# Kernel optimization log

Measured on AMD Instinct MI355X. Metric: run time of the kernel, lower is better.

The kernel has to match this reference:

```python
import jax, jax.numpy as jnp
import numpy as np

RADIUS = 1.3
COARSE = 64
FINE = 2
N_ATOMS = 64
SH_DIM = 9
DATA_DIM = SH_DIM * 3 + 1  # 28
N_INTRS = COARSE * 3 * 2 * FINE  # 768
STEP = (RADIUS * 2.0 / COARSE / FINE) / 2.0
BATCH = 1024


def sh_basis(d):
    # real spherical harmonics basis, degree 2 (9 coeffs), on normalized dirs
    d = d / jnp.linalg.norm(d, axis=-1, keepdims=True)
    x, y, z = d[..., 0], d[..., 1], d[..., 2]
    C0 = 0.28209479177387814
    C1 = 0.4886025119029199
    C20, C21, C22, C23, C24 = (1.0925484305920792, -1.0925484305920792,
                               0.31539156525252005, -1.0925484305920792,
                               0.5462742152960396)
    return jnp.stack([
        C0 * jnp.ones_like(x), -C1 * y, C1 * z, -C1 * x,
        C20 * x * y, C21 * y * z, C22 * (2.0 * z * z - x * x - y * y),
        C23 * x * z, C24 * (x * x - y * y)
    ], axis=-1)


def dict_interp(grid, atoms, pts):
    # l2_interp_v2: coarse-voxel dictionary coeffs x trilinear fine-atom interp
    # pts: [P,3] in [0,1)
    P = pts.shape[0]
    pc = pts * COARSE
    c = jnp.clip(jnp.floor(pc), 0, COARSE - 1).astype(jnp.int32)
    local = pc - c.astype(pts.dtype)  # position inside coarse voxel, [0,1)
    clin = (c[:, 0] * COARSE + c[:, 1]) * COARSE + c[:, 2]
    coeff = grid[clin]                              # [P, A]
    # project dictionary coeffs through atoms for every fine cell: [P, FINE^3, D]
    proj = jnp.einsum('pa,fad->pfd', coeff, atoms)
    u = local * FINE - 0.5
    f = jnp.floor(u)
    t = u - f
    i0 = jnp.clip(f, 0, FINE - 1).astype(jnp.int32)
    i1 = jnp.clip(f + 1.0, 0, FINE - 1).astype(jnp.int32)
    idx = jnp.stack([i0, i1], axis=-1)              # [P,3,2]
    w = jnp.stack([1.0 - t, t], axis=-1)            # [P,3,2]
    rows = jnp.arange(P)
    out = jnp.zeros((P, DATA_DIM), dtype=pts.dtype)
    for kx in (0, 1):
        for ky in (0, 1):
            for kz in (0, 1):
                lin = (idx[:, 0, kx] * FINE + idx[:, 1, ky]) * FINE + idx[:, 2, kz]
                wgt = w[:, 0, kx] * w[:, 1, ky] * w[:, 2, kz]
                out = out + wgt[:, None] * proj[rows, lin]
    return out


def _forward(rays_o, rays_d, grid, atoms):
    dt = rays_o.dtype
    # ---- sample_proposal (no grad) ----
    off_pos = (RADIUS - rays_o) / rays_d
    off_neg = (-RADIUS - rays_o) / rays_d
    start = jnp.max(jnp.minimum(off_pos, off_neg), axis=-1, keepdims=True)
    intersections = jax.lax.stop_gradient(
        start + jnp.arange(N_INTRS, dtype=dt)[None, :] * STEP)  # [B, 768]
    tr = intersections[:, :-1]  # [B, 767]
    pts = rays_o[:, None, :] + tr[..., None] * rays_d[:, None, :]  # [B,n,3]
    mask = jnp.all((pts > -RADIUS) & (pts < RADIUS), axis=-1)      # [B,n]
    pts = jax.lax.stop_gradient(pts)
    B, n = tr.shape
    # normalized coords in [0,1); masked-out points are clipped then zeroed later
    p = jnp.clip((pts + RADIUS) / (2.0 * RADIUS), 0.0, 1.0 - 1e-6).reshape(-1, 3)
    data = dict_interp(grid, atoms, p).reshape(B, n, DATA_DIM)
    # masked_scatter of sigma <=> dense compute + where(mask, ., 0)
    sigma = jnp.where(mask, jax.nn.relu(data[..., -1]), 0.0)
    dists = (intersections[:, 1:] - intersections[:, :-1]) * \
        jnp.linalg.norm(rays_d, axis=-1, keepdims=True)
    alpha = 1.0 - jnp.exp(-sigma * dists)
    trans = jnp.cumprod(1.0 - alpha + 1e-10, axis=-1)
    trans = jnp.concatenate([jnp.ones_like(trans[:, :1]), trans[:, :-1]], axis=-1)
    abs_light = alpha * trans  # per-sample weights
    sh_mult = sh_basis(rays_d)                      # [B, 9]
    sh = data[..., :-1].reshape(B, n, 3, SH_DIM)
    rgb_samp = jnp.einsum('bnck,bk->bnc', sh, sh_mult)
    rgb_samp = jax.nn.sigmoid(jnp.where(mask[..., None], rgb_samp, 0.0))
    comp = jnp.sum(abs_light[..., None] * rgb_samp, axis=1)  # [B,3]
    acc = jnp.sum(abs_light, axis=1)
    rgb = comp + (1.0 - acc)[:, None]  # white background
    depth = jnp.sum(abs_light * tr, axis=1)
    return rgb, alpha, depth


def setup_inputs():
    key = jax.random.key(0)
    k0, k1, k2, k3 = jax.random.split(key, 4)
    o = jax.random.normal(k0, (BATCH, 3), dtype=jnp.float32)
    o = o / jnp.linalg.norm(o, axis=-1, keepdims=True) * 2.5
    d = -o + 0.3 * jax.random.normal(k1, (BATCH, 3), dtype=jnp.float32)
    d = d / jnp.linalg.norm(d, axis=-1, keepdims=True)
    grid = 0.01 * jax.random.normal(k2, (COARSE ** 3, N_ATOMS), dtype=jnp.float32)
    atoms_sh = jax.random.uniform(k3, (FINE ** 3, N_ATOMS, DATA_DIM - 1), dtype=jnp.float32)
    atoms = jnp.concatenate(
        [atoms_sh, jnp.full((FINE ** 3, N_ATOMS, 1), 0.01, dtype=jnp.float32)], axis=-1)
    return {"rays_o": o, "rays_d": d, "grid": grid, "atoms": atoms, "grid_id": 0}


def reference(rays_o, rays_d, grid, atoms, grid_id):
    # grid_id selects among num_scenes grids; num_scenes=1 so grid is pre-selected
    return _forward(rays_o, rays_d, grid, atoms)
```

## Files before the change

kernel.cpp:

```cpp
#include <hip/hip_runtime.h>
#include <hip/hip_bf16.h>

#define RADIUS_F 1.3f
#define NSAMP 767
#define STEPF 0.01015625f
#define BATCH 1024
#define NWAVES 8
#define TPW 6

typedef __attribute__((ext_vector_type(8))) short short8;
typedef __attribute__((ext_vector_type(4))) float floatx4;

static __device__ __forceinline__ unsigned pkbf(float a, float b) {
    union { __hip_bfloat162 h; unsigned u; } cvt;
    cvt.h = __float22bfloat162_rn(make_float2(a, b));
    return cvt.u;
}

static __device__ __forceinline__ float coset4_sum(float p) {
    int q4 = __builtin_amdgcn_update_dpp(0, __float_as_int(p), 0x124, 0xf, 0xf, true);
    p = p + __int_as_float(q4);
    int q8 = __builtin_amdgcn_update_dpp(0, __float_as_int(p), 0x128, 0xf, 0xf, true);
    return p + __int_as_float(q8);
}

__launch_bounds__(512, 2)
__global__ void plenoxels_fwd(const float* __restrict__ rays_o,
                              const float* __restrict__ rays_d,
                              const float* __restrict__ grid,
                              const float* __restrict__ atoms,
                              float* __restrict__ out)
{
    __shared__ __align__(16) __hip_bfloat16 BpL[32 * 64];
    __shared__ __align__(16) float WL[NWAVES][16 * 12];
    __shared__ __align__(16) __hip_bfloat16 alphaL[768];
    __shared__ __align__(16) __hip_bfloat16 rgbL[768 * 3];

    const int tid  = threadIdx.x;
    const int ray  = blockIdx.x;
    const int lane = tid & 63;
    const int w    = tid >> 6;
    const int m    = lane & 15;
    const int quad = lane >> 4;

    const float ox = rays_o[ray * 3 + 0], oy = rays_o[ray * 3 + 1], oz = rays_o[ray * 3 + 2];
    const float dx = rays_d[ray * 3 + 0], dy = rays_d[ray * 3 + 1], dz = rays_d[ray * 3 + 2];

    float start;
    {
        float a0 = (RADIUS_F - ox) / dx, b0 = (-RADIUS_F - ox) / dx;
        float a1 = (RADIUS_F - oy) / dy, b1 = (-RADIUS_F - oy) / dy;
        float a2 = (RADIUS_F - oz) / dz, b2 = (-RADIUS_F - oz) / dz;
        start = fmaxf(fminf(a0, b0), fmaxf(fminf(a1, b1), fminf(a2, b2)));
    }
    const float dnorm = sqrtf(dx * dx + dy * dy + dz * dz);
    const float dist = STEPF * dnorm;

    float shm[9];
    {
        float inv = 1.0f / dnorm;
        float nx = dx * inv, ny = dy * inv, nz = dz * inv;
        shm[0] = 0.28209479177387814f;
        shm[1] = -0.4886025119029199f * ny;
        shm[2] = 0.4886025119029199f * nz;
        shm[3] = -0.4886025119029199f * nx;
        shm[4] = 1.0925484305920792f * nx * ny;
        shm[5] = -1.0925484305920792f * ny * nz;
        shm[6] = 0.31539156525252005f * (2.f * nz * nz - nx * nx - ny * ny);
        shm[7] = -1.0925484305920792f * nx * nz;
        shm[8] = 0.5462742152960396f * (nx * nx - ny * ny);
    }

    auto geom = [&](int s, float4& WA, float4& WB, int& clin) {
        float tr = start + (float)s * STEPF;
        float px = ox + tr * dx, py = oy + tr * dy, pz = oz + tr * dz;
        int mask = (px > -RADIUS_F) & (px < RADIUS_F) &
                   (py > -RADIUS_F) & (py < RADIUS_F) &
                   (pz > -RADIUS_F) & (pz < RADIUS_F);
        float maskf = mask ? 1.f : 0.f;
        const float sc = 1.0f / (2.0f * RADIUS_F);
        float qx = fminf(fmaxf((px + RADIUS_F) * sc, 0.f), 1.0f - 1e-6f);
        float qy = fminf(fmaxf((py + RADIUS_F) * sc, 0.f), 1.0f - 1e-6f);
        float qz = fminf(fmaxf((pz + RADIUS_F) * sc, 0.f), 1.0f - 1e-6f);
        float pcx = qx * 64.f, pcy = qy * 64.f, pcz = qz * 64.f;
        float cx = fminf(floorf(pcx), 63.f);
        float cy = fminf(floorf(pcy), 63.f);
        float cz = fminf(floorf(pcz), 63.f);
        float lx = pcx - cx, ly = pcy - cy, lz = pcz - cz;
        clin = (((int)cx * 64) + (int)cy) * 64 + (int)cz;
        float xw0, xw1, yw0, yw1, zw0, zw1;
        {
            float u = lx * 2.f - 0.5f, fF = floorf(u), t = u - fF;
            xw0 = (fF < 0.f) ? 1.f : ((fF > 0.f) ? 0.f : 1.f - t);
            xw1 = (fF < 0.f) ? 0.f : ((fF > 0.f) ? 1.f : t);
        }
        {
            float u = ly * 2.f - 0.5f, fF = floorf(u), t = u - fF;
            yw0 = (fF < 0.f) ? 1.f : ((fF > 0.f) ? 0.f : 1.f - t);
            yw1 = (fF < 0.f) ? 0.f : ((fF > 0.f) ? 1.f : t);
        }
        {
            float u = lz * 2.f - 0.5f, fF = floorf(u), t = u - fF;
            zw0 = (fF < 0.f) ? 1.f : ((fF > 0.f) ? 0.f : 1.f - t);
            zw1 = (fF < 0.f) ? 0.f : ((fF > 0.f) ? 1.f : t);
        }
        xw0 *= maskf; xw1 *= maskf;
        WA = make_float4(xw0 * yw0 * zw0, xw0 * yw0 * zw1, xw0 * yw1 * zw0, xw0 * yw1 * zw1);
        WB = make_float4(xw1 * yw0 * zw0, xw1 * yw0 * zw1, xw1 * yw1 * zw0, xw1 * yw1 * zw1);
    };

    const float4* g4 = (const float4*)grid;

    float4 WAc, WBc; int clinC;
    geom(w * (TPW * 16) + m, WAc, WBc, clinC);
    float4 cv0, cv1, cv2, cv3;
    {
        const float4* gp = g4 + (clinC << 4) + (quad << 2);
        cv0 = gp[0]; cv1 = gp[1]; cv2 = gp[2]; cv3 = gp[3];
    }

    for (int idx = tid; idx < 2048; idx += 512) {
        int col = idx >> 6, a = idx & 63;
        int f = col >> 2, c = col & 3;
        const float* base = atoms + (f * 64 + a) * 28;
        float sv;
        if (c == 3) sv = base[27];
        else {
            sv = 0.f;
            #pragma unroll
            for (int i = 0; i < 9; ++i) sv = fmaf(base[c * 9 + i], shm[i], sv);
        }
        BpL[col * 64 + a] = __float2bfloat16(sv);
    }
    __syncthreads();

    short8 bq00, bq01, bq10, bq11;
    {
        const short* bs = (const short*)BpL;
        const short* p0 = bs + m * 64 + (quad << 4);
        bq00 = *(const short8*)(p0);
        bq01 = *(const short8*)(p0 + 8);
        const short* p1 = bs + (16 + m) * 64 + (quad << 4);
        bq10 = *(const short8*)(p1);
        bq11 = *(const short8*)(p1 + 8);
    }

    float* out_rgb   = out;
    float* out_alpha = out + BATCH * 3;
    float* out_depth = out + BATCH * 3 + BATCH * NSAMP;

    for (int t = 0; t < TPW; ++t) {
        const int tile = w * TPW + t;

        if (quad == 0) {
            float* wrow = &WL[w][m * 12];
            *(float4*)(wrow)     = WAc;
            *(float4*)(wrow + 4) = WBc;
        }

        union { unsigned u[4]; short8 s; } a0, a1;
        a0.u[0] = pkbf(cv0.x, cv0.y); a0.u[1] = pkbf(cv0.z, cv0.w);
        a0.u[2] = pkbf(cv1.x, cv1.y); a0.u[3] = pkbf(cv1.z, cv1.w);
        a1.u[0] = pkbf(cv2.x, cv2.y); a1.u[1] = pkbf(cv2.z, cv2.w);
        a1.u[2] = pkbf(cv3.x, cv3.y); a1.u[3] = pkbf(cv3.z, cv3.w);

        if (t < TPW - 1) {
            geom(w * (TPW * 16) + (t + 1) * 16 + m, WAc, WBc, clinC);
            const float4* gp = g4 + (clinC << 4) + (quad << 2);
            cv0 = gp[0]; cv1 = gp[1]; cv2 = gp[2]; cv3 = gp[3];
        }

        floatx4 acc0 = {0.f, 0.f, 0.f, 0.f};
        floatx4 acc1 = {0.f, 0.f, 0.f, 0.f};
        acc0 = __builtin_amdgcn_mfma_f32_16x16x32_bf16(a0.s, bq00, acc0, 0, 0, 0);
        acc0 = __builtin_amdgcn_mfma_f32_16x16x32_bf16(a1.s, bq01, acc0, 0, 0, 0);
        acc1 = __builtin_amdgcn_mfma_f32_16x16x32_bf16(a0.s, bq10, acc1, 0, 0, 0);
        acc1 = __builtin_amdgcn_mfma_f32_16x16x32_bf16(a1.s, bq11, acc1, 0, 0, 0);

        const int f0 = m >> 2;
        #pragma unroll
        for (int r = 0; r < 4; ++r) {
            const float* wrow = &WL[w][((quad << 2) + r) * 12];
            float wA = wrow[f0];
            float wB = wrow[4 + f0];
            float p = wA * acc0[r] + wB * acc1[r];
            p = coset4_sum(p);
            int s = (tile << 4) + (quad << 2) + r;
            if (s < NSAMP) {
                if (m == 3) {
                    float al = 1.f - __expf(-fmaxf(p, 0.f) * dist);
                    out_alpha[ray * NSAMP + s] = al;
                    alphaL[s] = __float2bfloat16(al);
                } else if (m < 3) {
                    rgbL[s * 3 + m] = __float2bfloat16(1.f / (1.f + __expf(-p)));
                }
            }
        }
    }

    __syncthreads();

    if (tid < 64) {
        int sA = tid * 12;
        int sB = min(sA + 12, NSAMP);
        float prod = 1.f;
        for (int s = sA; s < sB; ++s)
            prod *= (1.f - __bfloat162float(alphaL[s]) + 1e-10f);

        float incl = prod;
        #pragma unroll
        for (int off = 1; off < 64; off <<= 1) {
            float v = __shfl_up(incl, off, 64);
            if (tid >= off) incl *= v;
        }
        float excl = __shfl_up(incl, 1, 64);
        if (tid == 0) excl = 1.f;

        float trans = excl;
        float c0 = 0.f, c1 = 0.f, c2 = 0.f, acc = 0.f, dep = 0.f;
        for (int s = sA; s < sB; ++s) {
            float a = __bfloat162float(alphaL[s]);
            float wgt = a * trans;
            c0 += wgt * __bfloat162float(rgbL[s * 3 + 0]);
            c1 += wgt * __bfloat162float(rgbL[s * 3 + 1]);
            c2 += wgt * __bfloat162float(rgbL[s * 3 + 2]);
            acc += wgt;
            dep += wgt * (start + (float)s * STEPF);
            trans *= (1.f - a + 1e-10f);
        }
        #pragma unroll
        for (int off = 1; off < 64; off <<= 1) {
            c0  += __shfl_xor(c0, off, 64);
            c1  += __shfl_xor(c1, off, 64);
            c2  += __shfl_xor(c2, off, 64);
            acc += __shfl_xor(acc, off, 64);
            dep += __shfl_xor(dep, off, 64);
        }
        if (tid == 0) {
            float bg = 1.f - acc;
            out_rgb[ray * 3 + 0] = c0 + bg;
            out_rgb[ray * 3 + 1] = c1 + bg;
            out_rgb[ray * 3 + 2] = c2 + bg;
            out_depth[ray] = dep;
        }
    }
}

extern "C" void kernel_launch(void* const* d_in, const int* in_sizes, int n_in,
                              void* d_out, int out_size, void* d_ws, size_t ws_size,
                              hipStream_t stream) {
    const float* rays_o = (const float*)d_in[0];
    const float* rays_d = (const float*)d_in[1];
    const float* grid   = (const float*)d_in[2];
    const float* atoms  = (const float*)d_in[3];
    float* out = (float*)d_out;
    hipLaunchKernelGGL(plenoxels_fwd, dim3(BATCH), dim3(512), 0, stream,
                       rays_o, rays_d, grid, atoms, out);
}
```

Measured before the change: 123.6 us.

## Compute sample geometry once per lane and share weights via LDS

The geometry and trilinear-weight computation now runs once per sample across all 64 lanes up front, instead of being repeated redundantly by each quad inside the tile loop. The eight weights per sample are stored in a block-wide shared array with stride 9, and the coarse-voxel indices are passed to the MFMA lanes with wave shuffles. The tile loop is fully unrolled and the launch-bounds occupancy hint is raised from 2 to 8. Costs: more LDS per block, possible bank conflicts on the stride-9 weight reads, and register pressure or spills if the compiler honours the higher occupancy hint.

```diff
diff --git a/kernel.cpp b/kernel.cpp
--- a/kernel.cpp
+++ b/kernel.cpp
@@ -5,8 +5,6 @@
 #define NSAMP 767
 #define STEPF 0.01015625f
 #define BATCH 1024
-#define NWAVES 8
-#define TPW 6
 
 typedef __attribute__((ext_vector_type(8))) short short8;
 typedef __attribute__((ext_vector_type(4))) float floatx4;
@@ -24,7 +22,7 @@
     return p + __int_as_float(q8);
 }
 
-__launch_bounds__(512, 2)
+__launch_bounds__(512, 8)
 __global__ void plenoxels_fwd(const float* __restrict__ rays_o,
                               const float* __restrict__ rays_d,
                               const float* __restrict__ grid,
@@ -32,7 +30,7 @@
                               float* __restrict__ out)
 {
     __shared__ __align__(16) __hip_bfloat16 BpL[32 * 64];
-    __shared__ __align__(16) float WL[NWAVES][16 * 12];
+    __shared__ float Wf[768 * 9];
     __shared__ __align__(16) __hip_bfloat16 alphaL[768];
     __shared__ __align__(16) __hip_bfloat16 rgbL[768 * 3];
 
@@ -56,8 +54,66 @@
     const float dnorm = sqrtf(dx * dx + dy * dy + dz * dz);
     const float dist = STEPF * dnorm;
 
-    float shm[9];
-    {
+    auto geom = [&](int s) -> int {
+        float tr = start + (float)s * STEPF;
+        float px = ox + tr * dx, py = oy + tr * dy, pz = oz + tr * dz;
+        int mask = (px > -RADIUS_F) & (px < RADIUS_F) &
+                   (py > -RADIUS_F) & (py < RADIUS_F) &
+                   (pz > -RADIUS_F) & (pz < RADIUS_F) & (s < NSAMP);
+        float maskf = mask ? 1.f : 0.f;
+        const float sc = 1.0f / (2.0f * RADIUS_F);
+        float qx = fminf(fmaxf((px + RADIUS_F) * sc, 0.f), 1.0f - 1e-6f);
+        float qy = fminf(fmaxf((py + RADIUS_F) * sc, 0.f), 1.0f - 1e-6f);
+        float qz = fminf(fmaxf((pz + RADIUS_F) * sc, 0.f), 1.0f - 1e-6f);
+        float pcx = qx * 64.f, pcy = qy * 64.f, pcz = qz * 64.f;
+        float cx = fminf(floorf(pcx), 63.f);
+        float cy = fminf(floorf(pcy), 63.f);
+        float cz = fminf(floorf(pcz), 63.f);
+        float lx = pcx - cx, ly = pcy - cy, lz = pcz - cz;
+        int clin = (((int)cx * 64) + (int)cy) * 64 + (int)cz;
+        float xw0, xw1, yw0, yw1, zw0, zw1;
+        {
+            float u = lx * 2.f - 0.5f, fF = floorf(u), t = u - fF;
+            xw0 = (fF < 0.f) ? 1.f : ((fF > 0.f) ? 0.f : 1.f - t);
+            xw1 = (fF < 0.f) ? 0.f : ((fF > 0.f) ? 1.f : t);
+        }
+        {
+            float u = ly * 2.f - 0.5f, fF = floorf(u), t = u - fF;
+            yw0 = (fF < 0.f) ? 1.f : ((fF > 0.f) ? 0.f : 1.f - t);
+            yw1 = (fF < 0.f) ? 0.f : ((fF > 0.f) ? 1.f : t);
+        }
+        {
+            float u = lz * 2.f - 0.5f, fF = floorf(u), t = u - fF;
+            zw0 = (fF < 0.f) ? 1.f : ((fF > 0.f) ? 0.f : 1.f - t);
+            zw1 = (fF < 0.f) ? 0.f : ((fF > 0.f) ? 1.f : t);
+        }
+        xw0 *= maskf; xw1 *= maskf;
+        float* wr = &Wf[s * 9];
+        wr[0] = xw0 * yw0 * zw0;
+        wr[1] = xw0 * yw0 * zw1;
+        wr[2] = xw0 * yw1 * zw0;
+        wr[3] = xw0 * yw1 * zw1;
+        wr[4] = xw1 * yw0 * zw0;
+        wr[5] = xw1 * yw0 * zw1;
+        wr[6] = xw1 * yw1 * zw0;
+        wr[7] = xw1 * yw1 * zw1;
+        return clin;
+    };
+
+    int clinA = geom(w * 96 + lane);
+    int clinB = 0;
+    if (lane < 32) clinB = geom(w * 96 + 64 + lane);
+
+    const float4* g4 = (const float4*)grid;
+    float4 cv0, cv1, cv2, cv3;
+    {
+        int clinC = __shfl(clinA, m, 64);
+        const float4* gp = g4 + (clinC << 4) + (quad << 2);
+        cv0 = gp[0]; cv1 = gp[1]; cv2 = gp[2]; cv3 = gp[3];
+    }
+
+    {
+        float shm[9];
         float inv = 1.0f / dnorm;
         float nx = dx * inv, ny = dy * inv, nz = dz * inv;
         shm[0] = 0.28209479177387814f;
@@ -69,68 +125,19 @@
         shm[6] = 0.31539156525252005f * (2.f * nz * nz - nx * nx - ny * ny);
         shm[7] = -1.0925484305920792f * nx * nz;
         shm[8] = 0.5462742152960396f * (nx * nx - ny * ny);
-    }
-
-    auto geom = [&](int s, float4& WA, float4& WB, int& clin) {
-        float tr = start + (float)s * STEPF;
-        float px = ox + tr * dx, py = oy + tr * dy, pz = oz + tr * dz;
-        int mask = (px > -RADIUS_F) & (px < RADIUS_F) &
-                   (py > -RADIUS_F) & (py < RADIUS_F) &
-                   (pz > -RADIUS_F) & (pz < RADIUS_F);
-        float maskf = mask ? 1.f : 0.f;
-        const float sc = 1.0f / (2.0f * RADIUS_F);
-        float qx = fminf(fmaxf((px + RADIUS_F) * sc, 0.f), 1.0f - 1e-6f);
-        float qy = fminf(fmaxf((py + RADIUS_F) * sc, 0.f), 1.0f - 1e-6f);
-        float qz = fminf(fmaxf((pz + RADIUS_F) * sc, 0.f), 1.0f - 1e-6f);
-        float pcx = qx * 64.f, pcy = qy * 64.f, pcz = qz * 64.f;
-        float cx = fminf(floorf(pcx), 63.f);
-        float cy = fminf(floorf(pcy), 63.f);
-        float cz = fminf(floorf(pcz), 63.f);
-        float lx = pcx - cx, ly = pcy - cy, lz = pcz - cz;
-        clin = (((int)cx * 64) + (int)cy) * 64 + (int)cz;
-        float xw0, xw1, yw0, yw1, zw0, zw1;
-        {
-            float u = lx * 2.f - 0.5f, fF = floorf(u), t = u - fF;
-            xw0 = (fF < 0.f) ? 1.f : ((fF > 0.f) ? 0.f : 1.f - t);
-            xw1 = (fF < 0.f) ? 0.f : ((fF > 0.f) ? 1.f : t);
-        }
-        {
-            float u = ly * 2.f - 0.5f, fF = floorf(u), t = u - fF;
-            yw0 = (fF < 0.f) ? 1.f : ((fF > 0.f) ? 0.f : 1.f - t);
-            yw1 = (fF < 0.f) ? 0.f : ((fF > 0.f) ? 1.f : t);
-        }
-        {
-            float u = lz * 2.f - 0.5f, fF = floorf(u), t = u - fF;
-            zw0 = (fF < 0.f) ? 1.f : ((fF > 0.f) ? 0.f : 1.f - t);
-            zw1 = (fF < 0.f) ? 0.f : ((fF > 0.f) ? 1.f : t);
-        }
-        xw0 *= maskf; xw1 *= maskf;
-        WA = make_float4(xw0 * yw0 * zw0, xw0 * yw0 * zw1, xw0 * yw1 * zw0, xw0 * yw1 * zw1);
-        WB = make_float4(xw1 * yw0 * zw0, xw1 * yw0 * zw1, xw1 * yw1 * zw0, xw1 * yw1 * zw1);
-    };
-
-    const float4* g4 = (const float4*)grid;
-
-    float4 WAc, WBc; int clinC;
-    geom(w * (TPW * 16) + m, WAc, WBc, clinC);
-    float4 cv0, cv1, cv2, cv3;
-    {
-        const float4* gp = g4 + (clinC << 4) + (quad << 2);
-        cv0 = gp[0]; cv1 = gp[1]; cv2 = gp[2]; cv3 = gp[3];
-    }
-
-    for (int idx = tid; idx < 2048; idx += 512) {
-        int col = idx >> 6, a = idx & 63;
-        int f = col >> 2, c = col & 3;
-        const float* base = atoms + (f * 64 + a) * 28;
-        float sv;
-        if (c == 3) sv = base[27];
-        else {
-            sv = 0.f;
-            #pragma unroll
-            for (int i = 0; i < 9; ++i) sv = fmaf(base[c * 9 + i], shm[i], sv);
-        }
-        BpL[col * 64 + a] = __float2bfloat16(sv);
+        for (int idx = tid; idx < 2048; idx += 512) {
+            int col = idx >> 6, a = idx & 63;
+            int f = col >> 2, c = col & 3;
+            const float* base = atoms + (f * 64 + a) * 28;
+            float sv;
+            if (c == 3) sv = base[27];
+            else {
+                sv = 0.f;
+                #pragma unroll
+                for (int i = 0; i < 9; ++i) sv = fmaf(base[c * 9 + i], shm[i], sv);
+            }
+            BpL[col * 64 + a] = __float2bfloat16(sv);
+        }
     }
     __syncthreads();
 
@@ -148,24 +155,20 @@
     float* out_rgb   = out;
     float* out_alpha = out + BATCH * 3;
     float* out_depth = out + BATCH * 3 + BATCH * NSAMP;
-
-    for (int t = 0; t < TPW; ++t) {
-        const int tile = w * TPW + t;
-
-        if (quad == 0) {
-            float* wrow = &WL[w][m * 12];
-            *(float4*)(wrow)     = WAc;
-            *(float4*)(wrow + 4) = WBc;
-        }
-
+    const int f0 = m >> 2;
+
+    #pragma unroll
+    for (int t = 0; t < 6; ++t) {
         union { unsigned u[4]; short8 s; } a0, a1;
         a0.u[0] = pkbf(cv0.x, cv0.y); a0.u[1] = pkbf(cv0.z, cv0.w);
         a0.u[2] = pkbf(cv1.x, cv1.y); a0.u[3] = pkbf(cv1.z, cv1.w);
         a1.u[0] = pkbf(cv2.x, cv2.y); a1.u[1] = pkbf(cv2.z, cv2.w);
         a1.u[2] = pkbf(cv3.x, cv3.y); a1.u[3] = pkbf(cv3.z, cv3.w);
 
-        if (t < TPW - 1) {
-            geom(w * (TPW * 16) + (t + 1) * 16 + m, WAc, WBc, clinC);
+        if (t < 5) {
+            int tn = t + 1;
+            int clinC = (tn < 4) ? __shfl(clinA, (tn << 4) + m, 64)
+                                 : __shfl(clinB, ((tn - 4) << 4) + m, 64);
             const float4* gp = g4 + (clinC << 4) + (quad << 2);
             cv0 = gp[0]; cv1 = gp[1]; cv2 = gp[2]; cv3 = gp[3];
         }
@@ -177,15 +180,12 @@
         acc1 = __builtin_amdgcn_mfma_f32_16x16x32_bf16(a0.s, bq10, acc1, 0, 0, 0);
         acc1 = __builtin_amdgcn_mfma_f32_16x16x32_bf16(a1.s, bq11, acc1, 0, 0, 0);
 
-        const int f0 = m >> 2;
         #pragma unroll
         for (int r = 0; r < 4; ++r) {
-            const float* wrow = &WL[w][((quad << 2) + r) * 12];
-            float wA = wrow[f0];
-            float wB = wrow[4 + f0];
-            float p = wA * acc0[r] + wB * acc1[r];
+            int s = w * 96 + (t << 4) + (quad << 2) + r;
+            const float* wr = &Wf[s * 9];
+            float p = wr[f0] * acc0[r] + wr[4 + f0] * acc1[r];
             p = coset4_sum(p);
-            int s = (tile << 4) + (quad << 2) + r;
             if (s < NSAMP) {
                 if (m == 3) {
                     float al = 1.f - __expf(-fmaxf(p, 0.f) * dist);
```

After: 120.7 us. 1.02x faster.
